# Optimization experiments

Hardware: AMD Instinct MI355X
Metric: run time of the kernel (lower is better)

The kernel has to match this reference:

```python
import jax, jax.numpy as jnp
import numpy as np

INPUT_SIZE = 512
HIDDEN_SIZE = 512
FORGET_BIAS = 1.0
B, T = 256, 256


def _xavier_uniform(key, shape):
    fan_out, fan_in = shape
    bound = jnp.sqrt(6.0 / (fan_in + fan_out))
    return jax.random.uniform(key, shape, jnp.float32, -bound, bound)


def setup_inputs() -> dict:
    key = jax.random.key(0)
    k1, k2, k3 = jax.random.split(key, 3)
    H, I = HIDDEN_SIZE, INPUT_SIZE
    x = jax.random.normal(k1, (B, T, I), jnp.float32)
    h0 = jnp.zeros((1, B, H), jnp.float32)
    c0 = jnp.zeros((1, B, H), jnp.float32)
    W_ih = _xavier_uniform(k2, (4 * H, I))
    W_hh = _xavier_uniform(k3, (4 * H, H))
    # biases init to zero, then forget_bias added to [H:2H] of BOTH biases (as in source)
    b = jnp.zeros((4 * H,), jnp.float32).at[H:2 * H].add(FORGET_BIAS)
    return {"input_tensor": x, "h0": h0, "c0": c0,
            "W_ih": W_ih, "W_hh": W_hh, "b_ih": b, "b_hh": b}


def reference(input_tensor, h0, c0, W_ih, W_hh, b_ih, b_hh):
    H = HIDDEN_SIZE
    half = H // 2
    b_all = b_ih + b_hh  # [4H]
    # precompute input projections for all timesteps: [T, B, 4H]
    x_proj = jnp.einsum('bti,gi->tbg', input_tensor, W_ih) + b_all

    def step(carry, xg):
        h, c, m = carry
        gates = xg + h @ W_hh.T                      # [B, 4H]
        i, f, g, o = jnp.split(gates, 4, axis=-1)
        c = jax.nn.sigmoid(f) * c + jax.nn.sigmoid(i) * jnp.tanh(g)
        h = jax.nn.sigmoid(o) * jnp.tanh(c)
        m = jnp.maximum(m, h[:, :half])              # running max over first half
        out = jnp.concatenate([m, h[:, half:]], axis=0)  # torch.cat default dim=0 -> [2B, half]
        return (h, c, m), out

    h_init = h0[0]
    c_init = c0[0]
    m_init = jnp.full((h_init.shape[0], half), -jnp.inf, h_init.dtype)
    (h_n, c_n, _), outs = jax.lax.scan(step, (h_init, c_init, m_init), x_proj)
    all_out = jnp.transpose(outs, (1, 0, 2))         # [2B, T, half]
    return all_out, h_n[None], c_n[None]
```

## Files before the change

kernel.cpp:

```cpp
#include <hip/hip_runtime.h>
#include <cstdint>

#define B_SZ 256
#define T_SZ 256
#define I_SZ 512
#define H_SZ 512
#define HALF 256

typedef __attribute__((ext_vector_type(8))) __bf16 bf16x8;
typedef __attribute__((ext_vector_type(8))) short short8;
typedef __attribute__((ext_vector_type(4))) float f32x4;
typedef __attribute__((ext_vector_type(4))) unsigned int uint4v;

__device__ __forceinline__ unsigned short f2bf(float f) {
  unsigned int u = __float_as_uint(f);
  u = (u + 0x7FFFu + ((u >> 16) & 1u)) >> 16;
  return (unsigned short)u;
}

__device__ __forceinline__ float sigm(float x) {
  return __builtin_amdgcn_rcpf(1.f + __expf(-x));
}
__device__ __forceinline__ float tanh_(float x) {
  float ax = fabsf(x);
  float e = __expf(-2.f * ax);
  float r = (1.f - e) * __builtin_amdgcn_rcpf(1.f + e);
  return copysignf(r, x);
}

__global__ void cvt_f32_bf16(const float* __restrict__ src, unsigned short* __restrict__ dst) {
  long i = ((long)blockIdx.x * 256 + threadIdx.x) * 8;
  float4 a = *(const float4*)(src + i);
  float4 b = *(const float4*)(src + i + 4);
  unsigned int w0 = (unsigned)f2bf(a.x) | ((unsigned)f2bf(a.y) << 16);
  unsigned int w1 = (unsigned)f2bf(a.z) | ((unsigned)f2bf(a.w) << 16);
  unsigned int w2 = (unsigned)f2bf(b.x) | ((unsigned)f2bf(b.y) << 16);
  unsigned int w3 = (unsigned)f2bf(b.z) | ((unsigned)f2bf(b.w) << 16);
  uint4v v = {w0, w1, w2, w3};
  *(uint4v*)(dst + i) = v;
}

__global__ void cvt_h0_tag(const float* __restrict__ h0, unsigned long long* __restrict__ dst) {
  int i = blockIdx.x * 256 + threadIdx.x;
  unsigned int pw = (unsigned)f2bf(h0[2 * i]) | ((unsigned)f2bf(h0[2 * i + 1]) << 16);
  dst[i] = (unsigned long long)pw;
}

__global__ void pack_w(const float* __restrict__ Wih, const float* __restrict__ Whh,
                       unsigned short* __restrict__ wp, unsigned short* __restrict__ hp) {
  int id = blockIdx.x * 256 + threadIdx.x;
  int cid = id & 131071;
  const float* W = (id < 131072) ? Wih : Whh;
  unsigned short* D = (id < 131072) ? wp : hp;
  int l  = cid & 63;
  int ks = (cid >> 6) & 15;
  int nt = (cid >> 10) & 1;
  int w  = (cid >> 11) & 3;
  int hg = (cid >> 13) & 15;
  int row = w * 512 + hg * 32 + nt * 16 + (l & 15);
  int k0  = ks * 32 + (l >> 4) * 8;
  const float* src = W + (long)row * 512 + k0;
  unsigned int wd[4];
#pragma unroll
  for (int j = 0; j < 4; ++j) {
    unsigned int lo = f2bf(src[2 * j]);
    unsigned int hi = f2bf(src[2 * j + 1]);
    wd[j] = lo | (hi << 16);
  }
  uint4v v = {wd[0], wd[1], wd[2], wd[3]};
  *(uint4v*)(D + (long)cid * 8) = v;
}

template <int SCOPE>
__device__ __forceinline__ void poll_fetch(const unsigned long long* src,
                                           unsigned tag, int tid,
                                           unsigned int* hpad) {
  unsigned long long v[16];
#pragma unroll
  for (int i = 0; i < 16; ++i)
    v[i] = __hip_atomic_load(src + i * 256 + tid, __ATOMIC_RELAXED, SCOPE);
  bool redo = true;
  while (redo) {
    redo = false;
#pragma unroll
    for (int i = 0; i < 16; ++i) {
      if ((unsigned)(v[i] >> 32) != tag) {
        v[i] = __hip_atomic_load(src + i * 256 + tid, __ATOMIC_RELAXED, SCOPE);
        redo = true;
      }
    }
  }
#pragma unroll
  for (int i = 0; i < 16; ++i)
    hpad[i * 260 + tid] = (unsigned int)v[i];
}

template <int SCOPE>
__device__ __forceinline__ void st64(unsigned long long* p, unsigned long long v) {
  __hip_atomic_store(p, v, __ATOMIC_RELAXED, SCOPE);
}

__global__ __launch_bounds__(256, 1) void lstm_main(
    const unsigned short* __restrict__ xb,
    const float* __restrict__ c0,
    const float* __restrict__ b_ih, const float* __restrict__ b_hh,
    const unsigned short* __restrict__ wihp, const unsigned short* __restrict__ whhp,
    unsigned long long* __restrict__ hw64,
    unsigned long long* __restrict__ cnt64,
    float* __restrict__ out)
{
  const int tid  = threadIdx.x;
  const int lane = tid & 63;
  const int w    = tid >> 6;
  const int bg   = blockIdx.x & 15;
  const int hg   = blockIdx.x >> 4;
  const int s0   = hg * 32;
  const int q    = lane >> 4;
  const int c16  = lane & 15;

  __shared__ float glds[4 * 528];
  __shared__ unsigned int hpad[16 * 260];
  __shared__ int s_path;

  int xcd;
  asm volatile("s_getreg_b32 %0, hwreg(20, 0, 32)" : "=s"(xcd));
  xcd &= 15;
  if (tid == 0) {
    unsigned long long inc = 1ull << (8 * xcd);
    __hip_atomic_fetch_add(&cnt64[bg * 8], inc, __ATOMIC_RELAXED, __HIP_MEMORY_SCOPE_SYSTEM);
    unsigned long long m;
    do {
      __builtin_amdgcn_s_sleep(2);
      m = __hip_atomic_load(&cnt64[bg * 8], __ATOMIC_RELAXED, __HIP_MEMORY_SCOPE_SYSTEM);
    } while ((unsigned)((m * 0x0101010101010101ull) >> 56) < 16);
    s_path = (m == (16ull << (8 * xcd))) ? 1 : 0;
  }
  __syncthreads();
  const bool agent_path = (s_path != 0);

  bf16x8 wih[2][16], whh[2][16];
#pragma unroll
  for (int nt = 0; nt < 2; ++nt) {
#pragma unroll
    for (int ks = 0; ks < 16; ++ks) {
      int idc = ((hg * 4 + w) * 2 + nt) * 16 + ks;
      long off = ((long)(idc * 64 + lane)) * 8;
      wih[nt][ks] = __builtin_bit_cast(bf16x8, *(const short8*)(wihp + off));
      whh[nt][ks] = __builtin_bit_cast(bf16x8, *(const short8*)(whhp + off));
    }
  }

  const int jj  = tid & 31;
  const int bl0 = tid >> 5;
  const int bglob0 = bg * 16 + bl0;
  const int bglob1 = bglob0 + 8;
  float bias_v[4];
#pragma unroll
  for (int g = 0; g < 4; ++g)
    bias_v[g] = b_ih[g * 512 + s0 + jj] + b_hh[g * 512 + s0 + jj];
  float cst0 = c0[(long)bglob0 * H_SZ + s0 + jj];
  float cst1 = c0[(long)bglob1 * H_SZ + s0 + jj];
  float m0 = -INFINITY, m1 = -INFINITY;

  const unsigned short* xbase = xb + (long)(bg * 16 + c16) * T_SZ * I_SZ + q * 8;

#pragma unroll 1
  for (int t = 0; t < T_SZ; ++t) {
    f32x4 acc0 = {0.f, 0.f, 0.f, 0.f};
    f32x4 acc1 = {0.f, 0.f, 0.f, 0.f};

    const unsigned short* xt = xbase + (long)t * I_SZ;
#pragma unroll
    for (int ks = 0; ks < 16; ++ks) {
      bf16x8 a = __builtin_bit_cast(bf16x8, *(const short8*)(xt + ks * 32));
      acc0 = __builtin_amdgcn_mfma_f32_16x16x32_bf16(a, wih[0][ks], acc0, 0, 0, 0);
      acc1 = __builtin_amdgcn_mfma_f32_16x16x32_bf16(a, wih[1][ks], acc1, 0, 0, 0);
    }

    {
      const unsigned long long* src = hw64 + ((t + 1) & 1) * 65536 + bg * 4096;
      if (agent_path) poll_fetch<__HIP_MEMORY_SCOPE_AGENT>(src, (unsigned)t, tid, hpad);
      else            poll_fetch<__HIP_MEMORY_SCOPE_SYSTEM>(src, (unsigned)t, tid, hpad);
    }
    __syncthreads();

    const unsigned int* hrow = hpad + c16 * 260;
#pragma unroll
    for (int ks = 0; ks < 16; ++ks) {
      bf16x8 a = __builtin_bit_cast(bf16x8, *(const short8*)(hrow + ks * 16 + q * 4));
      acc0 = __builtin_amdgcn_mfma_f32_16x16x32_bf16(a, whh[0][ks], acc0, 0, 0, 0);
      acc1 = __builtin_amdgcn_mfma_f32_16x16x32_bf16(a, whh[1][ks], acc1, 0, 0, 0);
    }

#pragma unroll
    for (int r = 0; r < 4; ++r) {
      glds[w * 528 + (q * 4 + r) * 33 + c16]      = acc0[r];
      glds[w * 528 + (q * 4 + r) * 33 + 16 + c16] = acc1[r];
    }
    __syncthreads();

    float hv0, hv1;
#pragma unroll
    for (int it = 0; it < 2; ++it) {
      int b = bl0 + it * 8;
      float gi = glds[0 * 528 + b * 33 + jj] + bias_v[0];
      float gf = glds[1 * 528 + b * 33 + jj] + bias_v[1];
      float gg = glds[2 * 528 + b * 33 + jj] + bias_v[2];
      float go = glds[3 * 528 + b * 33 + jj] + bias_v[3];
      float& cs = it ? cst1 : cst0;
      cs = sigm(gf) * cs + sigm(gi) * tanh_(gg);
      float h = sigm(go) * tanh_(cs);
      if (it) hv1 = h; else hv0 = h;
    }
    {
      float po0 = __shfl_xor(hv0, 1);
      float po1 = __shfl_xor(hv1, 1);
      if (!(jj & 1)) {
        unsigned long long tagw = (unsigned long long)(t + 1) << 32;
        unsigned long long w0 = tagw | ((unsigned)f2bf(hv0) | ((unsigned)f2bf(po0) << 16));
        unsigned long long w1 = tagw | ((unsigned)f2bf(hv1) | ((unsigned)f2bf(po1) << 16));
        unsigned long long* d0 = hw64 + (t & 1) * 65536 + bg * 4096
                               + bl0 * 256 + (s0 >> 1) + (jj >> 1);
        if (agent_path) {
          st64<__HIP_MEMORY_SCOPE_AGENT>(d0, w0);
          st64<__HIP_MEMORY_SCOPE_AGENT>(d0 + 8 * 256, w1);
        } else {
          st64<__HIP_MEMORY_SCOPE_SYSTEM>(d0, w0);
          st64<__HIP_MEMORY_SCOPE_SYSTEM>(d0 + 8 * 256, w1);
        }
      }
    }

#pragma unroll
    for (int it = 0; it < 2; ++it) {
      int b   = bl0 + it * 8;
      int bgl = bg * 16 + b;
      float h = it ? hv1 : hv0;
      float& mm = it ? m1 : m0;
      if (hg < 8) {
        mm = fmaxf(mm, h);
        out[(long)bgl * (T_SZ * HALF) + t * HALF + s0 + jj] = mm;
      } else {
        out[(long)(256 + bgl) * (T_SZ * HALF) + t * HALF + (s0 - 256) + jj] = h;
      }
      if (t == T_SZ - 1) {
        float cs = it ? cst1 : cst0;
        out[33554432L + (long)bgl * H_SZ + s0 + jj] = h;
        out[33554432L + 131072L + (long)bgl * H_SZ + s0 + jj] = cs;
      }
    }
  }
}

extern "C" void kernel_launch(void* const* d_in, const int* in_sizes, int n_in,
                              void* d_out, int out_size, void* d_ws, size_t ws_size,
                              hipStream_t stream) {
  const float* x   = (const float*)d_in[0];
  const float* h0  = (const float*)d_in[1];
  const float* c0  = (const float*)d_in[2];
  const float* Wih = (const float*)d_in[3];
  const float* Whh = (const float*)d_in[4];
  const float* bih = (const float*)d_in[5];
  const float* bhh = (const float*)d_in[6];
  float* out = (float*)d_out;

  char* ws = (char*)d_ws;
  unsigned short* xb     = (unsigned short*)(ws);
  unsigned short* wihp   = (unsigned short*)(ws + 67108864);
  unsigned short* whhp   = (unsigned short*)(ws + 69206016);
  unsigned long long* hw = (unsigned long long*)(ws + 71303168);
  unsigned long long* cn = (unsigned long long*)(ws + 72351744);

  hipMemsetAsync(cn, 0, 4096, stream);
  cvt_f32_bf16<<<16384, 256, 0, stream>>>(x, xb);
  cvt_h0_tag<<<256, 256, 0, stream>>>(h0, hw + 65536);
  pack_w<<<1024, 256, 0, stream>>>(Wih, Whh, wihp, whhp);
  lstm_main<<<256, 256, 0, stream>>>(xb, c0, bih, bhh, wihp, whhp, hw, cn, out);
}
```

Baseline: 1.561 ms.

## Replace tagged per-word h polling with per-wave flags and prefetch next x

```diff
diff --git a/kernel.cpp b/kernel.cpp
--- a/kernel.cpp
+++ b/kernel.cpp
@@ -40,10 +40,9 @@
   *(uint4v*)(dst + i) = v;
 }
 
-__global__ void cvt_h0_tag(const float* __restrict__ h0, unsigned long long* __restrict__ dst) {
+__global__ void cvt_h0(const float* __restrict__ h0, unsigned int* __restrict__ dst) {
   int i = blockIdx.x * 256 + threadIdx.x;
-  unsigned int pw = (unsigned)f2bf(h0[2 * i]) | ((unsigned)f2bf(h0[2 * i + 1]) << 16);
-  dst[i] = (unsigned long long)pw;
+  dst[i] = (unsigned)f2bf(h0[2 * i]) | ((unsigned)f2bf(h0[2 * i + 1]) << 16);
 }
 
 __global__ void pack_w(const float* __restrict__ Wih, const float* __restrict__ Whh,
@@ -71,33 +70,19 @@
   *(uint4v*)(D + (long)cid * 8) = v;
 }
 
-template <int SCOPE>
-__device__ __forceinline__ void poll_fetch(const unsigned long long* src,
-                                           unsigned tag, int tid,
-                                           unsigned int* hpad) {
-  unsigned long long v[16];
-#pragma unroll
-  for (int i = 0; i < 16; ++i)
-    v[i] = __hip_atomic_load(src + i * 256 + tid, __ATOMIC_RELAXED, SCOPE);
-  bool redo = true;
-  while (redo) {
-    redo = false;
-#pragma unroll
-    for (int i = 0; i < 16; ++i) {
-      if ((unsigned)(v[i] >> 32) != tag) {
-        v[i] = __hip_atomic_load(src + i * 256 + tid, __ATOMIC_RELAXED, SCOPE);
-        redo = true;
-      }
-    }
-  }
-#pragma unroll
-  for (int i = 0; i < 16; ++i)
-    hpad[i * 260 + tid] = (unsigned int)v[i];
-}
-
-template <int SCOPE>
-__device__ __forceinline__ void st64(unsigned long long* p, unsigned long long v) {
-  __hip_atomic_store(p, v, __ATOMIC_RELAXED, SCOPE);
+__device__ __forceinline__ unsigned int ld_flag(const unsigned int* p, bool agent) {
+  return agent ? __hip_atomic_load(p, __ATOMIC_RELAXED, __HIP_MEMORY_SCOPE_AGENT)
+               : __hip_atomic_load(p, __ATOMIC_RELAXED, __HIP_MEMORY_SCOPE_SYSTEM);
+}
+__device__ __forceinline__ void st_pub(unsigned int* p, unsigned int v, bool agent) {
+  if (agent) __hip_atomic_store(p, v, __ATOMIC_RELAXED, __HIP_MEMORY_SCOPE_AGENT);
+  else       __hip_atomic_store(p, v, __ATOMIC_RELAXED, __HIP_MEMORY_SCOPE_SYSTEM);
+}
+__device__ __forceinline__ uint4v ld_q(const unsigned int* p, bool agent) {
+  uint4v r;
+  if (agent) asm volatile("global_load_dwordx4 %0, %1, off sc0"     : "=&v"(r) : "v"(p) : "memory");
+  else       asm volatile("global_load_dwordx4 %0, %1, off sc0 sc1" : "=&v"(r) : "v"(p) : "memory");
+  return r;
 }
 
 __global__ __launch_bounds__(256, 1) void lstm_main(
@@ -105,7 +90,8 @@
     const float* __restrict__ c0,
     const float* __restrict__ b_ih, const float* __restrict__ b_hh,
     const unsigned short* __restrict__ wihp, const unsigned short* __restrict__ whhp,
-    unsigned long long* __restrict__ hw64,
+    unsigned int* __restrict__ hw32,
+    unsigned int* __restrict__ flags,
     unsigned long long* __restrict__ cnt64,
     float* __restrict__ out)
 {
@@ -119,7 +105,7 @@
   const int c16  = lane & 15;
 
   __shared__ float glds[4 * 528];
-  __shared__ unsigned int hpad[16 * 260];
+  __shared__ __align__(16) unsigned int hpad[16 * 260];
   __shared__ int s_path;
 
   int xcd;
@@ -164,25 +150,51 @@
 
   const unsigned short* xbase = xb + (long)(bg * 16 + c16) * T_SZ * I_SZ + q * 8;
 
+  const int p  = tid >> 4;
+  const int wv = (tid >> 2) & 3;
+  const int cq = tid & 3;
+  const unsigned int* fp = flags + (bg * 16 + p) * 4 + wv;
+  unsigned int* myflag = flags + (bg * 16 + hg) * 4 + w;
+
+  bf16x8 xr[16];
+#pragma unroll
+  for (int ks = 0; ks < 16; ++ks)
+    xr[ks] = __builtin_bit_cast(bf16x8, *(const short8*)(xbase + ks * 32));
+
 #pragma unroll 1
   for (int t = 0; t < T_SZ; ++t) {
     f32x4 acc0 = {0.f, 0.f, 0.f, 0.f};
     f32x4 acc1 = {0.f, 0.f, 0.f, 0.f};
 
-    const unsigned short* xt = xbase + (long)t * I_SZ;
+    unsigned int fpe = ld_flag(fp, agent_path);
+
 #pragma unroll
     for (int ks = 0; ks < 16; ++ks) {
-      bf16x8 a = __builtin_bit_cast(bf16x8, *(const short8*)(xt + ks * 32));
+      bf16x8 a = xr[ks];
       acc0 = __builtin_amdgcn_mfma_f32_16x16x32_bf16(a, wih[0][ks], acc0, 0, 0, 0);
       acc1 = __builtin_amdgcn_mfma_f32_16x16x32_bf16(a, wih[1][ks], acc1, 0, 0, 0);
     }
 
     {
-      const unsigned long long* src = hw64 + ((t + 1) & 1) * 65536 + bg * 4096;
-      if (agent_path) poll_fetch<__HIP_MEMORY_SCOPE_AGENT>(src, (unsigned)t, tid, hpad);
-      else            poll_fetch<__HIP_MEMORY_SCOPE_SYSTEM>(src, (unsigned)t, tid, hpad);
-    }
-    __syncthreads();
+      while (fpe < (unsigned)t) { fpe = ld_flag(fp, agent_path); }
+      const unsigned int* src = hw32 + ((t + 1) & 1) * 65536 + bg * 4096 + p * 16 + cq * 4;
+      uint4v v0 = ld_q(src + (2 * wv)     * 256, agent_path);
+      uint4v v1 = ld_q(src + (2 * wv + 1) * 256, agent_path);
+      uint4v v2 = ld_q(src + (2 * wv + 8) * 256, agent_path);
+      uint4v v3 = ld_q(src + (2 * wv + 9) * 256, agent_path);
+      const unsigned short* xn = xbase + (long)(t + 1 < T_SZ ? t + 1 : t) * I_SZ;
+#pragma unroll
+      for (int ks = 0; ks < 16; ++ks)
+        xr[ks] = __builtin_bit_cast(bf16x8, *(const short8*)(xn + ks * 32));
+      asm volatile("s_waitcnt vmcnt(16)" ::: "memory");
+      *(uint4v*)(hpad + (2 * wv)     * 260 + p * 16 + cq * 4) = v0;
+      *(uint4v*)(hpad + (2 * wv + 1) * 260 + p * 16 + cq * 4) = v1;
+      *(uint4v*)(hpad + (2 * wv + 8) * 260 + p * 16 + cq * 4) = v2;
+      *(uint4v*)(hpad + (2 * wv + 9) * 260 + p * 16 + cq * 4) = v3;
+      asm volatile("s_waitcnt lgkmcnt(0)" ::: "memory");
+      __builtin_amdgcn_s_barrier();
+      asm volatile("" ::: "memory");
+    }
 
     const unsigned int* hrow = hpad + c16 * 260;
 #pragma unroll
@@ -216,19 +228,15 @@
       float po0 = __shfl_xor(hv0, 1);
       float po1 = __shfl_xor(hv1, 1);
       if (!(jj & 1)) {
-        unsigned long long tagw = (unsigned long long)(t + 1) << 32;
-        unsigned long long w0 = tagw | ((unsigned)f2bf(hv0) | ((unsigned)f2bf(po0) << 16));
-        unsigned long long w1 = tagw | ((unsigned)f2bf(hv1) | ((unsigned)f2bf(po1) << 16));
-        unsigned long long* d0 = hw64 + (t & 1) * 65536 + bg * 4096
-                               + bl0 * 256 + (s0 >> 1) + (jj >> 1);
-        if (agent_path) {
-          st64<__HIP_MEMORY_SCOPE_AGENT>(d0, w0);
-          st64<__HIP_MEMORY_SCOPE_AGENT>(d0 + 8 * 256, w1);
-        } else {
-          st64<__HIP_MEMORY_SCOPE_SYSTEM>(d0, w0);
-          st64<__HIP_MEMORY_SCOPE_SYSTEM>(d0 + 8 * 256, w1);
-        }
+        unsigned int w0 = (unsigned)f2bf(hv0) | ((unsigned)f2bf(po0) << 16);
+        unsigned int w1 = (unsigned)f2bf(hv1) | ((unsigned)f2bf(po1) << 16);
+        unsigned int* d0 = hw32 + (t & 1) * 65536 + bg * 4096
+                         + bl0 * 256 + (s0 >> 1) + (jj >> 1);
+        st_pub(d0, w0, agent_path);
+        st_pub(d0 + 8 * 256, w1, agent_path);
       }
+      asm volatile("s_waitcnt vmcnt(0)" ::: "memory");
+      if (lane == 0) st_pub(myflag, (unsigned)(t + 1), agent_path);
     }
 
 #pragma unroll
@@ -265,15 +273,16 @@
   float* out = (float*)d_out;
 
   char* ws = (char*)d_ws;
-  unsigned short* xb     = (unsigned short*)(ws);
-  unsigned short* wihp   = (unsigned short*)(ws + 67108864);
-  unsigned short* whhp   = (unsigned short*)(ws + 69206016);
-  unsigned long long* hw = (unsigned long long*)(ws + 71303168);
-  unsigned long long* cn = (unsigned long long*)(ws + 72351744);
-
-  hipMemsetAsync(cn, 0, 4096, stream);
+  unsigned short* xb   = (unsigned short*)(ws);
+  unsigned short* wihp = (unsigned short*)(ws + 67108864);
+  unsigned short* whhp = (unsigned short*)(ws + 69206016);
+  unsigned int* hw     = (unsigned int*)(ws + 71303168);
+  unsigned long long* cn = (unsigned long long*)(ws + 71827456);
+  unsigned int* fl     = (unsigned int*)(ws + 71831552);
+
+  hipMemsetAsync(cn, 0, 8192, stream);
   cvt_f32_bf16<<<16384, 256, 0, stream>>>(x, xb);
-  cvt_h0_tag<<<256, 256, 0, stream>>>(h0, hw + 65536);
+  cvt_h0<<<256, 256, 0, stream>>>(h0, hw + 65536);
   pack_w<<<1024, 256, 0, stream>>>(Wih, Whh, wihp, whhp);
-  lstm_main<<<256, 256, 0, stream>>>(xb, c0, bih, bhh, wihp, whhp, hw, cn, out);
-}
+  lstm_main<<<256, 256, 0, stream>>>(xb, c0, bih, bhh, wihp, whhp, hw, fl, cn, out);
+}
```

New measurement: 1.654 ms. 1.06x slower.

## Prefetch next-step x and issue h polls before input MFMAs with swizzled LDS

Applied to the files above, without the earlier changes.

```diff
diff --git a/kernel.cpp b/kernel.cpp
--- a/kernel.cpp
+++ b/kernel.cpp
@@ -40,10 +40,11 @@
   *(uint4v*)(dst + i) = v;
 }
 
-__global__ void cvt_h0_tag(const float* __restrict__ h0, unsigned long long* __restrict__ dst) {
+__global__ void init_hw(const float* __restrict__ h0, unsigned long long* __restrict__ dst) {
   int i = blockIdx.x * 256 + threadIdx.x;
   unsigned int pw = (unsigned)f2bf(h0[2 * i]) | ((unsigned)f2bf(h0[2 * i + 1]) << 16);
-  dst[i] = (unsigned long long)pw;
+  dst[65536 + i] = (unsigned long long)pw;
+  dst[i] = 0xFFFFFFFF00000000ull;
 }
 
 __global__ void pack_w(const float* __restrict__ Wih, const float* __restrict__ Whh,
@@ -71,28 +72,29 @@
   *(uint4v*)(D + (long)cid * 8) = v;
 }
 
+#define LDPA(dst, base, OFFSTR) \
+  asm volatile("global_load_dwordx2 %0, %1, off offset:" OFFSTR " sc0" : "=v"(dst) : "v"(base))
+#define LDPS(dst, base, OFFSTR) \
+  asm volatile("global_load_dwordx2 %0, %1, off offset:" OFFSTR " sc0 sc1" : "=v"(dst) : "v"(base))
+#define LDX16(dst, base, OFFSTR) \
+  asm volatile("global_load_dwordx4 %0, %1, off offset:" OFFSTR : "=v"(dst) : "v"(base))
+
 template <int SCOPE>
-__device__ __forceinline__ void poll_fetch(const unsigned long long* src,
-                                           unsigned tag, int tid,
-                                           unsigned int* hpad) {
-  unsigned long long v[16];
-#pragma unroll
-  for (int i = 0; i < 16; ++i)
-    v[i] = __hip_atomic_load(src + i * 256 + tid, __ATOMIC_RELAXED, SCOPE);
+__device__ __forceinline__ void poll_check(unsigned long long* pv,
+                                           const unsigned long long* srcb,
+                                           int wv, unsigned tag) {
   bool redo = true;
   while (redo) {
     redo = false;
 #pragma unroll
     for (int i = 0; i < 16; ++i) {
-      if ((unsigned)(v[i] >> 32) != tag) {
-        v[i] = __hip_atomic_load(src + i * 256 + tid, __ATOMIC_RELAXED, SCOPE);
+      if ((unsigned)(pv[i] >> 32) != tag) {
+        const int row = 2 * wv + ((i >> 2) & 1) + (i >> 3) * 8;
+        pv[i] = __hip_atomic_load(srcb + row * 256 + (i & 3), __ATOMIC_RELAXED, SCOPE);
         redo = true;
       }
     }
   }
-#pragma unroll
-  for (int i = 0; i < 16; ++i)
-    hpad[i * 260 + tid] = (unsigned int)v[i];
 }
 
 template <int SCOPE>
@@ -119,7 +121,7 @@
   const int c16  = lane & 15;
 
   __shared__ float glds[4 * 528];
-  __shared__ unsigned int hpad[16 * 260];
+  __shared__ __align__(16) unsigned int hpad[16 * 260];
   __shared__ int s_path;
 
   int xcd;
@@ -164,30 +166,96 @@
 
   const unsigned short* xbase = xb + (long)(bg * 16 + c16) * T_SZ * I_SZ + q * 8;
 
+  const int p   = tid >> 4;
+  const int wv  = (tid >> 2) & 3;
+  const int cq  = tid & 3;
+  const int colbase = p * 16 + cq * 4;
+
+  const int swz = (c16 & 7) << 2;
+
+  bf16x8 xr[16];
+  {
+    const unsigned short* xn = xbase;
+    LDX16(xr[0],  xn, "0");   LDX16(xr[1],  xn, "64");
+    LDX16(xr[2],  xn, "128"); LDX16(xr[3],  xn, "192");
+    LDX16(xr[4],  xn, "256"); LDX16(xr[5],  xn, "320");
+    LDX16(xr[6],  xn, "384"); LDX16(xr[7],  xn, "448");
+    LDX16(xr[8],  xn, "512"); LDX16(xr[9],  xn, "576");
+    LDX16(xr[10], xn, "640"); LDX16(xr[11], xn, "704");
+    LDX16(xr[12], xn, "768"); LDX16(xr[13], xn, "832");
+    LDX16(xr[14], xn, "896"); LDX16(xr[15], xn, "960");
+  }
+
 #pragma unroll 1
   for (int t = 0; t < T_SZ; ++t) {
+    asm volatile("s_waitcnt vmcnt(0)" ::: "memory");
+    __builtin_amdgcn_sched_barrier(0);
+
+    const unsigned long long* srcb = hw64 + ((t + 1) & 1) * 65536 + bg * 4096 + colbase;
+    const unsigned long long* blo = srcb + 2 * wv * 256;
+    const unsigned long long* bhi = blo + 8 * 256;
+    unsigned long long pv[16];
+    if (agent_path) {
+      LDPA(pv[0],  blo, "0");    LDPA(pv[1],  blo, "8");
+      LDPA(pv[2],  blo, "16");   LDPA(pv[3],  blo, "24");
+      LDPA(pv[4],  blo, "2048"); LDPA(pv[5],  blo, "2056");
+      LDPA(pv[6],  blo, "2064"); LDPA(pv[7],  blo, "2072");
+      LDPA(pv[8],  bhi, "0");    LDPA(pv[9],  bhi, "8");
+      LDPA(pv[10], bhi, "16");   LDPA(pv[11], bhi, "24");
+      LDPA(pv[12], bhi, "2048"); LDPA(pv[13], bhi, "2056");
+      LDPA(pv[14], bhi, "2064"); LDPA(pv[15], bhi, "2072");
+    } else {
+      LDPS(pv[0],  blo, "0");    LDPS(pv[1],  blo, "8");
+      LDPS(pv[2],  blo, "16");   LDPS(pv[3],  blo, "24");
+      LDPS(pv[4],  blo, "2048"); LDPS(pv[5],  blo, "2056");
+      LDPS(pv[6],  blo, "2064"); LDPS(pv[7],  blo, "2072");
+      LDPS(pv[8],  bhi, "0");    LDPS(pv[9],  bhi, "8");
+      LDPS(pv[10], bhi, "16");   LDPS(pv[11], bhi, "24");
+      LDPS(pv[12], bhi, "2048"); LDPS(pv[13], bhi, "2056");
+      LDPS(pv[14], bhi, "2064"); LDPS(pv[15], bhi, "2072");
+    }
+
     f32x4 acc0 = {0.f, 0.f, 0.f, 0.f};
     f32x4 acc1 = {0.f, 0.f, 0.f, 0.f};
-
-    const unsigned short* xt = xbase + (long)t * I_SZ;
 #pragma unroll
     for (int ks = 0; ks < 16; ++ks) {
-      bf16x8 a = __builtin_bit_cast(bf16x8, *(const short8*)(xt + ks * 32));
+      bf16x8 a = xr[ks];
       acc0 = __builtin_amdgcn_mfma_f32_16x16x32_bf16(a, wih[0][ks], acc0, 0, 0, 0);
       acc1 = __builtin_amdgcn_mfma_f32_16x16x32_bf16(a, wih[1][ks], acc1, 0, 0, 0);
     }
 
+    asm volatile("s_waitcnt vmcnt(0)" ::: "memory");
+    __builtin_amdgcn_sched_barrier(0);
+
+    if (agent_path) poll_check<__HIP_MEMORY_SCOPE_AGENT>(pv, srcb, wv, (unsigned)t);
+    else            poll_check<__HIP_MEMORY_SCOPE_SYSTEM>(pv, srcb, wv, (unsigned)t);
+#pragma unroll
+    for (int g = 0; g < 4; ++g) {
+      const int row = 2 * wv + (g & 1) + (g >> 1) * 8;
+      const int pc  = colbase ^ ((row & 7) << 2);
+      uint4v d = {(unsigned int)pv[g * 4 + 0], (unsigned int)pv[g * 4 + 1],
+                  (unsigned int)pv[g * 4 + 2], (unsigned int)pv[g * 4 + 3]};
+      *(uint4v*)(hpad + row * 260 + pc) = d;
+    }
+    __syncthreads();
+
     {
-      const unsigned long long* src = hw64 + ((t + 1) & 1) * 65536 + bg * 4096;
-      if (agent_path) poll_fetch<__HIP_MEMORY_SCOPE_AGENT>(src, (unsigned)t, tid, hpad);
-      else            poll_fetch<__HIP_MEMORY_SCOPE_SYSTEM>(src, (unsigned)t, tid, hpad);
-    }
-    __syncthreads();
+      const unsigned short* xn = xbase + (long)(t + 1 < T_SZ ? t + 1 : t) * I_SZ;
+      LDX16(xr[0],  xn, "0");   LDX16(xr[1],  xn, "64");
+      LDX16(xr[2],  xn, "128"); LDX16(xr[3],  xn, "192");
+      LDX16(xr[4],  xn, "256"); LDX16(xr[5],  xn, "320");
+      LDX16(xr[6],  xn, "384"); LDX16(xr[7],  xn, "448");
+      LDX16(xr[8],  xn, "512"); LDX16(xr[9],  xn, "576");
+      LDX16(xr[10], xn, "640"); LDX16(xr[11], xn, "704");
+      LDX16(xr[12], xn, "768"); LDX16(xr[13], xn, "832");
+      LDX16(xr[14], xn, "896"); LDX16(xr[15], xn, "960");
+    }
 
     const unsigned int* hrow = hpad + c16 * 260;
 #pragma unroll
     for (int ks = 0; ks < 16; ++ks) {
-      bf16x8 a = __builtin_bit_cast(bf16x8, *(const short8*)(hrow + ks * 16 + q * 4));
+      bf16x8 a = __builtin_bit_cast(bf16x8,
+                   *(const short8*)(hrow + ((ks * 16 + q * 4) ^ swz)));
       acc0 = __builtin_amdgcn_mfma_f32_16x16x32_bf16(a, whh[0][ks], acc0, 0, 0, 0);
       acc1 = __builtin_amdgcn_mfma_f32_16x16x32_bf16(a, whh[1][ks], acc1, 0, 0, 0);
     }
@@ -273,7 +341,7 @@
 
   hipMemsetAsync(cn, 0, 4096, stream);
   cvt_f32_bf16<<<16384, 256, 0, stream>>>(x, xb);
-  cvt_h0_tag<<<256, 256, 0, stream>>>(h0, hw + 65536);
+  init_hw<<<256, 256, 0, stream>>>(h0, hw);
   pack_w<<<1024, 256, 0, stream>>>(Wih, Whh, wihp, whhp);
   lstm_main<<<256, 256, 0, stream>>>(xb, c0, bih, bhh, wihp, whhp, hw, cn, out);
 }
```

Measured after the change: 1.401 ms. -10.3%, faster.
